# Kernel optimization log

Hardware: AMD Instinct MI355X
Metric: run time of the kernel (lower is better)

Reference implementation:

```python
import jax, jax.numpy as jnp
import numpy as np

B, N, F_IN, HID, HEADS, LAYERS = 512, 128, 128, 64, 4, 3
NEG_SLOPE = 0.2  # DenseGATConv default


def setup_inputs() -> dict:
    key = jax.random.key(0)
    ks = jax.random.split(key, 1 + 4 * LAYERS)
    inp = {}
    inp["x"] = jax.random.normal(ks[0], (B * N, F_IN), jnp.float32)
    # uniform graph sizes: graph i owns nodes [i*N, (i+1)*N)
    inp["batch_mask"] = jnp.repeat(jnp.arange(B, dtype=jnp.int32), N)
    dims = [F_IN] + [HID * HEADS] * (LAYERS - 1)
    for l in range(LAYERS):
        d = dims[l]
        k = 4 * l
        inp[f"W{l}"] = jax.random.normal(ks[1 + k], (d, HEADS * HID), jnp.float32) / np.sqrt(d)
        inp[f"att_src{l}"] = jax.random.normal(ks[2 + k], (HEADS, HID), jnp.float32) * 0.1
        inp[f"att_dst{l}"] = jax.random.normal(ks[3 + k], (HEADS, HID), jnp.float32) * 0.1
        inp[f"b{l}"] = jnp.zeros((HEADS * HID,), jnp.float32)  # zero-init bias, as in PyG
    return inp


def _dense_gat(x, adj, W, att_src, att_dst, bias):
    # x: [B, N, F_in], adj: [N, N] (shared structure, broadcast over batch)
    b, n, _ = x.shape
    h = (x @ W).reshape(b, n, HEADS, HID)                       # [B,N,H,C]
    a_src = jnp.einsum('bnhc,hc->bnh', h, att_src)              # [B,N,H]
    a_dst = jnp.einsum('bnhc,hc->bnh', h, att_dst)              # [B,N,H]
    # alpha[b,i,j,h] = a_src[b,j,h] + a_dst[b,i,h]
    alpha = a_src[:, None, :, :] + a_dst[:, :, None, :]         # [B,N,N,H]
    alpha = jnp.where(alpha >= 0, alpha, NEG_SLOPE * alpha)
    alpha = jnp.where(adj[None, :, :, None] == 0, -jnp.inf, alpha)
    alpha = jax.nn.softmax(alpha, axis=2)                       # softmax over sources j
    out = jnp.einsum('bijh,bjhc->bihc', alpha, h)               # [B,N,H,C]
    return out.reshape(b, n, HEADS * HID) + bias                # concat heads + bias


def reference(x, batch_mask, W0, att_src0, att_dst0, b0,
              W1, att_src1, att_dst1, b1, W2, att_src2, att_dst2, b2):
    # to_dense_batch with uniform graph sizes == reshape; batch_mask encodes this layout
    h = x.reshape(B, N, F_IN)
    eye = jnp.eye(N, dtype=x.dtype)
    # GNNBlock builds full adjacency with zeroed diagonal ...
    adj = jnp.ones((N, N), x.dtype) - eye
    # ... and DenseGATConv(add_loop=True) re-adds self-loops
    adj = jnp.maximum(adj, eye)
    params = [(W0, att_src0, att_dst0, b0), (W1, att_src1, att_dst1, b1),
              (W2, att_src2, att_dst2, b2)]
    for (W, a_s, a_d, b) in params:
        h = _dense_gat(h, adj, W, a_s, a_d, b)
        # block act is nn.LeakyReLU(True): negative_slope=True==1.0 -> identity
        h = jnp.where(h >= 0, h, 1.0 * h)
    return h.sum(axis=1)  # [B, HEADS*HID]
```

## Files before the change

kernel.cpp:

```cpp
#include <hip/hip_runtime.h>
#include <hip/hip_bf16.h>


typedef unsigned short u16;
typedef __attribute__((ext_vector_type(8))) short short8;
typedef __attribute__((ext_vector_type(4))) float f32x4;

#define L2E 1.44269504088896340736f

__device__ __forceinline__ u16 f2bf(float f) {
  unsigned int u = __float_as_uint(f);
  u += 0x7fffu + ((u >> 16) & 1u);
  return (u16)(u >> 16);
}
__device__ __forceinline__ unsigned int pk2(float a, float b) {
  __hip_bfloat162 h2 = __float22bfloat162_rn(make_float2(a, b));
  unsigned int u;
  __builtin_memcpy(&u, &h2, 4);
  return u;
}

__device__ __forceinline__ int xs_byte(int row, int col) {
  return (row << 9) + ((col << 1) ^ ((row & 7) << 4));
}
__device__ __forceinline__ int ht_byte(int row, int col) {
  return (row << 8) + ((col << 1) ^ ((row & 7) << 4));
}

__global__ void prep_w(const float* __restrict__ W0, const float* __restrict__ W1,
                       const float* __restrict__ W2,
                       const float* __restrict__ as0, const float* __restrict__ ad0,
                       const float* __restrict__ as1, const float* __restrict__ ad1,
                       const float* __restrict__ as2, const float* __restrict__ ad2,
                       u16* __restrict__ wt) {
  const int bid = blockIdx.x, tid = threadIdx.x;
  if (bid < 80) {
    const float* W; int NKB, base, rel;
    if (bid < 16)      { W = W0; NKB = 4; base = 0;      rel = bid; }
    else if (bid < 48) { W = W1; NKB = 8; base = 34816;  rel = bid - 16; }
    else               { W = W2; NKB = 8; base = 104448; rel = bid - 48; }
    const int kb = rel >> 2, ko = rel & 3;
    const int n = tid;
    union { u16 v[8]; short8 s; } u;
    #pragma unroll
    for (int e = 0; e < 8; ++e)
      u.v[e] = f2bf(W[(kb * 32 + ko * 8 + e) * 256 + n]);
    const int t = n >> 4, l15 = n & 15;
    *(short8*)(wt + base + (((t * NKB + kb) * 64 + l15 + (ko << 4)) << 3)) = u.s;
  } else if (bid < 100) {
    int b2 = bid - 80;
    const float* W; const float* as; const float* ad; int NKB, base, kb;
    if (b2 < 4)       { W = W0; as = as0; ad = ad0; NKB = 4; base = 0;      kb = b2; }
    else if (b2 < 12) { W = W1; as = as1; ad = ad1; NKB = 8; base = 34816;  kb = b2 - 4; }
    else              { W = W2; as = as2; ad = ad2; NKB = 8; base = 104448; kb = b2 - 12; }
    const int kloc = tid >> 3, col = tid & 7, h = col & 3;
    const int k = kb * 32 + kloc;
    const float* av = (col < 4) ? as : ad;
    float acc = 0.f;
    #pragma unroll 8
    for (int c = 0; c < 64; ++c)
      acc = fmaf(W[k * 256 + h * 64 + c], av[h * 64 + c], acc);
    const int lane2 = col + ((kloc >> 3) << 4), e = kloc & 7;
    const int tb = base + ((16 * NKB + kb) << 9);
    wt[tb + ((lane2) << 3) + e]     = f2bf(acc);
    wt[tb + ((lane2 + 8) << 3) + e] = 0;
  }
}

__global__ __launch_bounds__(1024, 4) void gat_all(
    const float* __restrict__ x, const u16* __restrict__ wt,
    const float* __restrict__ bb0, const float* __restrict__ bb1,
    const float* __restrict__ bb2, float* __restrict__ out)
{
  constexpr int XS = 0;
  constexpr int HT = 65536;
  constexpr int SB = 131072;
  constexpr int DB = 133120;
  constexpr int PM = 135168;
  constexpr int BS = 135232;
  constexpr int OA = 136256;
  __shared__ unsigned char smem[137280];

  float* sbuf  = (float*)(smem + SB);
  float* dbuf  = (float*)(smem + DB);
  float* pmaxw = (float*)(smem + PM);
  float* bsb   = (float*)(smem + BS);
  float* oac   = (float*)(smem + OA);

  const int b    = blockIdx.x;
  const int tid  = threadIdx.x;
  const int w    = tid >> 6;
  const int lane = tid & 63;
  const int l15  = lane & 15;
  const int lg   = lane >> 4;

  {
    const float4* xg = (const float4*)(x + (size_t)b * (128 * 128));
    #pragma unroll
    for (int it = 0; it < 4; ++it) {
      int e = tid + it * 1024;
      float4 v = xg[e];
      int row = e >> 5, c = (e & 31) << 2;
      uint2 u = { pk2(v.x, v.y), pk2(v.z, v.w) };
      *(uint2*)(smem + XS + xs_byte(row, c)) = u;
    }
  }
  __syncthreads();

  const u16* wfl[3]    = {wt, wt + 34816, wt + 104448};
  const float* bias[3] = {bb0, bb1, bb2};

  #pragma unroll
  for (int l = 0; l < 3; ++l) {
    const int NKB = (l == 0) ? 4 : 8;
    const u16* wf = wfl[l];

    if (tid < 256) {
      bsb[tid] = bias[l][tid];
      if (l == 2) oac[tid] = 0.f;
    }
    {
      const int mw = w & 1, nw = w >> 1;
      f32x4 acc[4][2] = {};
      for (int ks = 0; ks < NKB; ++ks) {
        const int kcol = ks * 32 + lg * 8;
        short8 afr[4];
        #pragma unroll
        for (int mi = 0; mi < 4; ++mi)
          afr[mi] = *(const short8*)(smem + XS + xs_byte(mw * 64 + mi * 16 + l15, kcol));
        short8 bfr[2];
        #pragma unroll
        for (int ni = 0; ni < 2; ++ni) {
          int t = nw * 2 + ni;
          bfr[ni] = *(const short8*)(wf + (((t * NKB + ks) * 64 + lane) << 3));
        }
        #pragma unroll
        for (int mi = 0; mi < 4; ++mi)
          #pragma unroll
          for (int ni = 0; ni < 2; ++ni)
            acc[mi][ni] = __builtin_amdgcn_mfma_f32_16x16x32_bf16(
                afr[mi], bfr[ni], acc[mi][ni], 0, 0, 0);
      }
      #pragma unroll
      for (int mi = 0; mi < 4; ++mi) {
        int j0 = mw * 64 + mi * 16 + lg * 4;
        #pragma unroll
        for (int ni = 0; ni < 2; ++ni) {
          int c = nw * 32 + ni * 16 + l15;
          uint2 u = { pk2(acc[mi][ni][0], acc[mi][ni][1]),
                      pk2(acc[mi][ni][2], acc[mi][ni][3]) };
          *(uint2*)(smem + HT + ht_byte(c, j0)) = u;
        }
      }
    }

    if (w >= 14) {
      const int mw = w & 1;
      f32x4 acc2[4] = {};
      for (int ks = 0; ks < NKB; ++ks) {
        const int kcol = ks * 32 + lg * 8;
        short8 bsd = *(const short8*)(wf + (((16 * NKB + ks) * 64 + lane) << 3));
        #pragma unroll
        for (int mi = 0; mi < 4; ++mi) {
          short8 a = *(const short8*)(smem + XS + xs_byte(mw * 64 + mi * 16 + l15, kcol));
          acc2[mi] = __builtin_amdgcn_mfma_f32_16x16x32_bf16(a, bsd, acc2[mi], 0, 0, 0);
        }
      }
      float mx = -3.4e38f;
      #pragma unroll
      for (int mi = 0; mi < 4; ++mi) {
        f32x4 v = acc2[mi] * L2E;
        if (l15 < 8) {
          float* basep = (float*)(smem + (l15 < 4 ? SB : DB))
                       + (l15 & 3) * 128 + mw * 64 + mi * 16 + lg * 4;
          *(float4*)basep = (float4){v[0], v[1], v[2], v[3]};
        }
        mx = fmaxf(mx, fmaxf(fmaxf(v[0], v[1]), fmaxf(v[2], v[3])));
      }
      mx = fmaxf(mx, __shfl_xor(mx, 16));
      mx = fmaxf(mx, __shfl_xor(mx, 32));
      if (lane < 4) pmaxw[lane * 2 + mw] = mx;
    }
    __syncthreads();

    {
      const int hw = w >> 2, q = w & 3;
      f32x4 acc[4][2] = {};
      float den[2] = {0.f, 0.f};
      float dvv[2], nml[2];
      int ib[2];
      const float smax = fmaxf(pmaxw[hw * 2], pmaxw[hw * 2 + 1]);
      #pragma unroll
      for (int ni = 0; ni < 2; ++ni) {
        int i = q * 32 + ni * 16 + l15;
        ib[ni] = hw * 128 + i;
        dvv[ni] = dbuf[ib[ni]];
        float tm = smax + dvv[ni];
        nml[ni] = -fmaxf(tm, 0.2f * tm);
      }
      #pragma unroll
      for (int ks = 0; ks < 4; ++ks) {
        const int j0 = ks * 32 + lg * 8;
        float sj[8];
        #pragma unroll
        for (int jj = 0; jj < 8; ++jj) sj[jj] = sbuf[hw * 128 + j0 + jj];
        short8 afr[4];
        #pragma unroll
        for (int mi = 0; mi < 4; ++mi)
          afr[mi] = *(const short8*)(smem + HT + ht_byte(hw * 64 + mi * 16 + l15, j0));
        short8 bfr[2];
        #pragma unroll
        for (int ni = 0; ni < 2; ++ni) {
          float e[8];
          #pragma unroll
          for (int jj = 0; jj < 8; ++jj) {
            float t = sj[jj] + dvv[ni];
            t = fmaxf(t, 0.2f * t);
            e[jj] = exp2f(t + nml[ni]);
          }
          den[ni] += ((e[0] + e[1]) + (e[2] + e[3])) + ((e[4] + e[5]) + (e[6] + e[7]));
          union { short8 s; unsigned int u[4]; } pk;
          #pragma unroll
          for (int t2 = 0; t2 < 4; ++t2) pk.u[t2] = pk2(e[2 * t2], e[2 * t2 + 1]);
          bfr[ni] = pk.s;
        }
        #pragma unroll
        for (int mi = 0; mi < 4; ++mi)
          #pragma unroll
          for (int ni = 0; ni < 2; ++ni)
            acc[mi][ni] = __builtin_amdgcn_mfma_f32_16x16x32_bf16(
                afr[mi], bfr[ni], acc[mi][ni], 0, 0, 0);
      }
      float rvv[2];
      #pragma unroll
      for (int ni = 0; ni < 2; ++ni) {
        float d2 = den[ni];
        d2 += __shfl_xor(d2, 16);
        d2 += __shfl_xor(d2, 32);
        rvv[ni] = 1.f / d2;
      }
      if (l < 2) {
        #pragma unroll
        for (int mi = 0; mi < 4; ++mi) {
          int c0 = hw * 64 + mi * 16 + lg * 4;
          float b0v = bsb[c0], b1v = bsb[c0 + 1], b2v = bsb[c0 + 2], b3v = bsb[c0 + 3];
          #pragma unroll
          for (int ni = 0; ni < 2; ++ni) {
            int i = q * 32 + ni * 16 + l15;
            float r = rvv[ni];
            uint2 u = { pk2(fmaf(acc[mi][ni][0], r, b0v), fmaf(acc[mi][ni][1], r, b1v)),
                        pk2(fmaf(acc[mi][ni][2], r, b2v), fmaf(acc[mi][ni][3], r, b3v)) };
            *(uint2*)(smem + XS + xs_byte(i, c0)) = u;
          }
        }
      } else {
        #pragma unroll
        for (int mi = 0; mi < 4; ++mi) {
          #pragma unroll
          for (int reg = 0; reg < 4; ++reg) {
            float pv2 = acc[mi][0][reg] * rvv[0] + acc[mi][1][reg] * rvv[1];
            pv2 += __shfl_xor(pv2, 1);
            pv2 += __shfl_xor(pv2, 2);
            pv2 += __shfl_xor(pv2, 4);
            pv2 += __shfl_xor(pv2, 8);
            if (l15 == 0)
              atomicAdd(&oac[hw * 64 + mi * 16 + lg * 4 + reg], pv2);
          }
        }
      }
    }
    __syncthreads();
  }

  if (tid < 256) out[(size_t)b * 256 + tid] = oac[tid] + 128.f * bsb[tid];
}

extern "C" void kernel_launch(void* const* d_in, const int* in_sizes, int n_in,
                              void* d_out, int out_size, void* d_ws, size_t ws_size,
                              hipStream_t stream) {
  const float* x   = (const float*)d_in[0];
  const float* W0  = (const float*)d_in[2];
  const float* as0 = (const float*)d_in[3];
  const float* ad0 = (const float*)d_in[4];
  const float* b0  = (const float*)d_in[5];
  const float* W1  = (const float*)d_in[6];
  const float* as1 = (const float*)d_in[7];
  const float* ad1 = (const float*)d_in[8];
  const float* b1  = (const float*)d_in[9];
  const float* W2  = (const float*)d_in[10];
  const float* as2 = (const float*)d_in[11];
  const float* ad2 = (const float*)d_in[12];
  const float* b2  = (const float*)d_in[13];
  u16* wt = (u16*)d_ws;

  hipLaunchKernelGGL(prep_w, dim3(100), dim3(256), 0, stream,
                     W0, W1, W2, as0, ad0, as1, ad1, as2, ad2, wt);
  hipLaunchKernelGGL(gat_all, dim3(512), dim3(1024), 0, stream,
                     x, wt, b0, b1, b2, (float*)d_out);
}
```

Baseline: 174.4 us.

## Alias X and H^T LDS buffers to halve shared memory and raise occupancy

Shared memory drops from about 137KB to 72KB by letting the bf16 X tile and the transposed H tile share one 64KB buffer. Extra __syncthreads barriers keep the aliasing safe: the projection result stays in registers until every wave has finished reading X, and a barrier before the output write protects H^T. With the smaller LDS footprint and launch bounds raised to 8, two 1024-thread blocks may fit per CU. The attention-score GEMM is also spread over 4 waves instead of 2, and sbuf reads are vectorized. The cost is two extra block-wide barriers per layer and more register pressure, since the projection accumulators stay live across a barrier.

New measurement: 280.5 us. +60.8%, slower.

```diff
diff --git a/kernel.cpp b/kernel.cpp
--- a/kernel.cpp
+++ b/kernel.cpp
@@ -67,19 +67,18 @@
   }
 }
 
-__global__ __launch_bounds__(1024, 4) void gat_all(
+__global__ __launch_bounds__(1024, 8) void gat_all(
     const float* __restrict__ x, const u16* __restrict__ wt,
     const float* __restrict__ bb0, const float* __restrict__ bb1,
     const float* __restrict__ bb2, float* __restrict__ out)
 {
-  constexpr int XS = 0;
-  constexpr int HT = 65536;
-  constexpr int SB = 131072;
-  constexpr int DB = 133120;
-  constexpr int PM = 135168;
-  constexpr int BS = 135232;
-  constexpr int OA = 136256;
-  __shared__ unsigned char smem[137280];
+  constexpr int AB = 0;
+  constexpr int SB = 65536;
+  constexpr int DB = 67584;
+  constexpr int PM = 69632;
+  constexpr int BS = 69696;
+  constexpr int OA = 70720;
+  __shared__ __align__(16) unsigned char smem[71744];
 
   float* sbuf  = (float*)(smem + SB);
   float* dbuf  = (float*)(smem + DB);
@@ -102,7 +101,7 @@
       float4 v = xg[e];
       int row = e >> 5, c = (e & 31) << 2;
       uint2 u = { pk2(v.x, v.y), pk2(v.z, v.w) };
-      *(uint2*)(smem + XS + xs_byte(row, c)) = u;
+      *(uint2*)(smem + AB + xs_byte(row, c)) = u;
     }
   }
   __syncthreads();
@@ -119,95 +118,96 @@
       bsb[tid] = bias[l][tid];
       if (l == 2) oac[tid] = 0.f;
     }
-    {
-      const int mw = w & 1, nw = w >> 1;
-      f32x4 acc[4][2] = {};
-      for (int ks = 0; ks < NKB; ++ks) {
-        const int kcol = ks * 32 + lg * 8;
-        short8 afr[4];
-        #pragma unroll
-        for (int mi = 0; mi < 4; ++mi)
-          afr[mi] = *(const short8*)(smem + XS + xs_byte(mw * 64 + mi * 16 + l15, kcol));
-        short8 bfr[2];
-        #pragma unroll
-        for (int ni = 0; ni < 2; ++ni) {
-          int t = nw * 2 + ni;
-          bfr[ni] = *(const short8*)(wf + (((t * NKB + ks) * 64 + lane) << 3));
-        }
-        #pragma unroll
-        for (int mi = 0; mi < 4; ++mi)
-          #pragma unroll
-          for (int ni = 0; ni < 2; ++ni)
-            acc[mi][ni] = __builtin_amdgcn_mfma_f32_16x16x32_bf16(
-                afr[mi], bfr[ni], acc[mi][ni], 0, 0, 0);
-      }
-      #pragma unroll
-      for (int mi = 0; mi < 4; ++mi) {
-        int j0 = mw * 64 + mi * 16 + lg * 4;
-        #pragma unroll
-        for (int ni = 0; ni < 2; ++ni) {
-          int c = nw * 32 + ni * 16 + l15;
-          uint2 u = { pk2(acc[mi][ni][0], acc[mi][ni][1]),
-                      pk2(acc[mi][ni][2], acc[mi][ni][3]) };
-          *(uint2*)(smem + HT + ht_byte(c, j0)) = u;
-        }
-      }
-    }
-
-    if (w >= 14) {
-      const int mw = w & 1;
-      f32x4 acc2[4] = {};
+
+    const int mw = w & 1, nw = w >> 1;
+    f32x4 acc[4][2] = {};
+    for (int ks = 0; ks < NKB; ++ks) {
+      const int kcol = ks * 32 + lg * 8;
+      short8 afr[4];
+      #pragma unroll
+      for (int mi = 0; mi < 4; ++mi)
+        afr[mi] = *(const short8*)(smem + AB + xs_byte(mw * 64 + mi * 16 + l15, kcol));
+      short8 bfr[2];
+      #pragma unroll
+      for (int ni = 0; ni < 2; ++ni) {
+        int t = nw * 2 + ni;
+        bfr[ni] = *(const short8*)(wf + (((t * NKB + ks) * 64 + lane) << 3));
+      }
+      #pragma unroll
+      for (int mi = 0; mi < 4; ++mi)
+        #pragma unroll
+        for (int ni = 0; ni < 2; ++ni)
+          acc[mi][ni] = __builtin_amdgcn_mfma_f32_16x16x32_bf16(
+              afr[mi], bfr[ni], acc[mi][ni], 0, 0, 0);
+    }
+
+    if (w >= 12) {
+      const int mw2 = w & 1, mih = (w >> 1) & 1;
+      f32x4 acc2[2] = {};
       for (int ks = 0; ks < NKB; ++ks) {
         const int kcol = ks * 32 + lg * 8;
         short8 bsd = *(const short8*)(wf + (((16 * NKB + ks) * 64 + lane) << 3));
         #pragma unroll
-        for (int mi = 0; mi < 4; ++mi) {
-          short8 a = *(const short8*)(smem + XS + xs_byte(mw * 64 + mi * 16 + l15, kcol));
-          acc2[mi] = __builtin_amdgcn_mfma_f32_16x16x32_bf16(a, bsd, acc2[mi], 0, 0, 0);
+        for (int mi2 = 0; mi2 < 2; ++mi2) {
+          short8 a = *(const short8*)(smem + AB +
+              xs_byte(mw2 * 64 + (mih * 2 + mi2) * 16 + l15, kcol));
+          acc2[mi2] = __builtin_amdgcn_mfma_f32_16x16x32_bf16(a, bsd, acc2[mi2], 0, 0, 0);
         }
       }
       float mx = -3.4e38f;
       #pragma unroll
-      for (int mi = 0; mi < 4; ++mi) {
-        f32x4 v = acc2[mi] * L2E;
+      for (int mi2 = 0; mi2 < 2; ++mi2) {
+        f32x4 v = acc2[mi2] * L2E;
         if (l15 < 8) {
           float* basep = (float*)(smem + (l15 < 4 ? SB : DB))
-                       + (l15 & 3) * 128 + mw * 64 + mi * 16 + lg * 4;
+                       + (l15 & 3) * 128 + mw2 * 64 + (mih * 2 + mi2) * 16 + lg * 4;
           *(float4*)basep = (float4){v[0], v[1], v[2], v[3]};
         }
         mx = fmaxf(mx, fmaxf(fmaxf(v[0], v[1]), fmaxf(v[2], v[3])));
       }
       mx = fmaxf(mx, __shfl_xor(mx, 16));
       mx = fmaxf(mx, __shfl_xor(mx, 32));
-      if (lane < 4) pmaxw[lane * 2 + mw] = mx;
+      if (lane < 4) pmaxw[lane * 4 + (w - 12)] = mx;
+    }
+    __syncthreads();
+
+    #pragma unroll
+    for (int mi = 0; mi < 4; ++mi) {
+      int j0 = mw * 64 + mi * 16 + lg * 4;
+      #pragma unroll
+      for (int ni = 0; ni < 2; ++ni) {
+        int c = nw * 32 + ni * 16 + l15;
+        uint2 u = { pk2(acc[mi][ni][0], acc[mi][ni][1]),
+                    pk2(acc[mi][ni][2], acc[mi][ni][3]) };
+        *(uint2*)(smem + AB + ht_byte(c, j0)) = u;
+      }
     }
     __syncthreads();
 
     {
       const int hw = w >> 2, q = w & 3;
-      f32x4 acc[4][2] = {};
+      f32x4 facc[4][2] = {};
       float den[2] = {0.f, 0.f};
       float dvv[2], nml[2];
-      int ib[2];
-      const float smax = fmaxf(pmaxw[hw * 2], pmaxw[hw * 2 + 1]);
+      const float smax = fmaxf(fmaxf(pmaxw[hw * 4], pmaxw[hw * 4 + 1]),
+                               fmaxf(pmaxw[hw * 4 + 2], pmaxw[hw * 4 + 3]));
       #pragma unroll
       for (int ni = 0; ni < 2; ++ni) {
         int i = q * 32 + ni * 16 + l15;
-        ib[ni] = hw * 128 + i;
-        dvv[ni] = dbuf[ib[ni]];
+        dvv[ni] = dbuf[hw * 128 + i];
         float tm = smax + dvv[ni];
         nml[ni] = -fmaxf(tm, 0.2f * tm);
       }
       #pragma unroll
       for (int ks = 0; ks < 4; ++ks) {
         const int j0 = ks * 32 + lg * 8;
-        float sj[8];
-        #pragma unroll
-        for (int jj = 0; jj < 8; ++jj) sj[jj] = sbuf[hw * 128 + j0 + jj];
+        float4 s03 = *(const float4*)(sbuf + hw * 128 + j0);
+        float4 s47 = *(const float4*)(sbuf + hw * 128 + j0 + 4);
+        float sj[8] = {s03.x, s03.y, s03.z, s03.w, s47.x, s47.y, s47.z, s47.w};
         short8 afr[4];
         #pragma unroll
         for (int mi = 0; mi < 4; ++mi)
-          afr[mi] = *(const short8*)(smem + HT + ht_byte(hw * 64 + mi * 16 + l15, j0));
+          afr[mi] = *(const short8*)(smem + AB + ht_byte(hw * 64 + mi * 16 + l15, j0));
         short8 bfr[2];
         #pragma unroll
         for (int ni = 0; ni < 2; ++ni) {
@@ -228,8 +228,8 @@
         for (int mi = 0; mi < 4; ++mi)
           #pragma unroll
           for (int ni = 0; ni < 2; ++ni)
-            acc[mi][ni] = __builtin_amdgcn_mfma_f32_16x16x32_bf16(
-                afr[mi], bfr[ni], acc[mi][ni], 0, 0, 0);
+            facc[mi][ni] = __builtin_amdgcn_mfma_f32_16x16x32_bf16(
+                afr[mi], bfr[ni], facc[mi][ni], 0, 0, 0);
       }
       float rvv[2];
       #pragma unroll
@@ -239,6 +239,8 @@
         d2 += __shfl_xor(d2, 32);
         rvv[ni] = 1.f / d2;
       }
+      __syncthreads();
+
       if (l < 2) {
         #pragma unroll
         for (int mi = 0; mi < 4; ++mi) {
@@ -248,9 +250,9 @@
           for (int ni = 0; ni < 2; ++ni) {
             int i = q * 32 + ni * 16 + l15;
             float r = rvv[ni];
-            uint2 u = { pk2(fmaf(acc[mi][ni][0], r, b0v), fmaf(acc[mi][ni][1], r, b1v)),
-                        pk2(fmaf(acc[mi][ni][2], r, b2v), fmaf(acc[mi][ni][3], r, b3v)) };
-            *(uint2*)(smem + XS + xs_byte(i, c0)) = u;
+            uint2 u = { pk2(fmaf(facc[mi][ni][0], r, b0v), fmaf(facc[mi][ni][1], r, b1v)),
+                        pk2(fmaf(facc[mi][ni][2], r, b2v), fmaf(facc[mi][ni][3], r, b3v)) };
+            *(uint2*)(smem + AB + xs_byte(i, c0)) = u;
           }
         }
       } else {
@@ -258,7 +260,7 @@
         for (int mi = 0; mi < 4; ++mi) {
           #pragma unroll
           for (int reg = 0; reg < 4; ++reg) {
-            float pv2 = acc[mi][0][reg] * rvv[0] + acc[mi][1][reg] * rvv[1];
+            float pv2 = facc[mi][0][reg] * rvv[0] + facc[mi][1][reg] * rvv[1];
             pv2 += __shfl_xor(pv2, 1);
             pv2 += __shfl_xor(pv2, 2);
             pv2 += __shfl_xor(pv2, 4);
```
